# Optimization experiments

Measured on AMD Instinct MI355X. Metric: run time of the kernel, lower is better.

## Reference

```python
import jax, jax.numpy as jnp
import numpy as np

N = 20000   # nodes per type per hop
E = 200000  # edges per relation per hop
H = 512     # node_feature_hid_len
FU = 512    # raw user feature len
FI = 256    # raw item feature len
NUM_RES = 2
NUM_DNN = 2


def setup_inputs() -> dict:
    key = jax.random.key(0)
    ks = iter(jax.random.split(key, 64))
    p = lambda shape: jax.random.normal(next(ks), shape, dtype=jnp.float32) * 0.05
    inp = {}
    # features per hop per type
    for h in range(3):
        inp[f'feat_user_h{h}'] = jax.random.normal(next(ks), (N, FU), dtype=jnp.float32)
        inp[f'feat_item_h{h}'] = jax.random.normal(next(ks), (N, FI), dtype=jnp.float32)
    del inp['feat_user_h2_']; 


def _unused():
    pass

# rebuild setup_inputs cleanly (above stub replaced)

def setup_inputs() -> dict:
    key = jax.random.key(0)
    ks = iter(jax.random.split(key, 64))
    p = lambda shape: jax.random.normal(next(ks), shape, dtype=jnp.float32) * 0.05
    inp = {}
    for h in range(3):
        inp[f'feat_user_h{h}'] = jax.random.normal(next(ks), (N, FU), dtype=jnp.float32)
        inp[f'feat_item_h{h}'] = jax.random.normal(next(ks), (N, FI), dtype=jnp.float32)
    for name in ('edges_UI_h0', 'edges_IU_h0', 'edges_UI_h1', 'edges_IU_h1'):
        inp[name] = jax.random.randint(next(ks), (2, E), 0, N, dtype=jnp.int32)
    # per-node-type input transforms
    inp['W_user'] = p((FU, H)); inp['b_user'] = jnp.zeros((H,), jnp.float32)
    inp['W_item'] = p((FI, H)); inp['b_item'] = jnp.zeros((H,), jnp.float32)
    # per-relation GATConv params, stacked over 2 relations [UI, IU]
    inp['gat_feat_W'] = p((2, H, H)); inp['gat_feat_b'] = jnp.zeros((2, H), jnp.float32)
    inp['gat_att_w'] = p((2, 2 * H)); inp['gat_att_b'] = jnp.zeros((2,), jnp.float32)
    inp['gat_bias'] = jnp.zeros((2, H), jnp.float32)
    # Res_DNN params
    inp['prep_W'] = p((H, H)); inp['prep_b'] = jnp.zeros((H,), jnp.float32)
    inp['dnn_W'] = p((NUM_RES, NUM_DNN, H, H)); inp['dnn_b'] = jnp.zeros((NUM_RES, NUM_DNN, H), jnp.float32)
    inp['dnn_ln_g'] = jnp.ones((NUM_RES, NUM_DNN, H), jnp.float32); inp['dnn_ln_b'] = jnp.zeros((NUM_RES, NUM_DNN, H), jnp.float32)
    inp['res_ln_g'] = jnp.ones((NUM_RES, H), jnp.float32); inp['res_ln_b'] = jnp.zeros((NUM_RES, H), jnp.float32)
    inp['cls_W'] = p((H, 1)); inp['cls_b'] = jnp.zeros((1,), jnp.float32)
    return inp


def _ln(x, g, b, eps=1e-5):
    mu = jnp.mean(x, axis=-1, keepdims=True)
    var = jnp.mean((x - mu) ** 2, axis=-1, keepdims=True)
    return (x - mu) * jax.lax.rsqrt(var + eps) * g + b


def _gat(head_h, tail_h, edges, fW, fb, aw, ab, bias):
    # GATConv: feat_linear on both sides, tanh edge attention, per-source-row
    # sparse softmax, scatter-weighted sum of transformed tail features.
    s = head_h @ fW + fb            # [Nh, H]
    t = tail_h @ fW + fb            # [Nt, H]
    src, tgt = edges[0], edges[1]
    # att(cat([s_e, t_e])) split into per-node scores (same math as concat @ aw)
    e = jnp.tanh((s @ aw[:H])[src] + (t @ aw[H:])[tgt] + ab)  # [E]
    nh = head_h.shape[0]
    m = jax.ops.segment_max(e, src, num_segments=nh)
    ex = jnp.exp(e - m[src])
    den = jax.ops.segment_sum(ex, src, num_segments=nh)
    alpha = ex / den[src]
    hp = jax.ops.segment_sum(alpha[:, None] * t[tgt], src, num_segments=nh)
    return hp + bias


def _forward(feat_user_h0, feat_item_h0, feat_user_h1, feat_item_h1,
             feat_user_h2, feat_item_h2,
             W_user, b_user, W_item, b_item,
             gat_feat_W, gat_feat_b, gat_att_w, gat_att_b, gat_bias,
             prep_W, prep_b, dnn_W, dnn_b, dnn_ln_g, dnn_ln_b,
             res_ln_g, res_ln_b, cls_W, cls_b,
             edges_UI_h0, edges_IU_h0, edges_UI_h1, edges_IU_h1):
    def gat(r, head, tail, edges):
        return _gat(head, tail, edges, gat_feat_W[r], gat_feat_b[r],
                    gat_att_w[r], gat_att_b[r], gat_bias[r])
    # hop 2 (deepest): transformed source features
    su = feat_user_h2 @ W_user + b_user
    si = feat_item_h2 @ W_item + b_item
    # hop 1
    hu = feat_user_h1 @ W_user + b_user
    hi = feat_item_h1 @ W_item + b_item
    su_new = (hu + gat(0, hu, si, edges_UI_h1)) * 0.5  # mean of [self, UI agg]
    si_new = (hi + gat(1, hi, su, edges_IU_h1)) * 0.5
    su, si = su_new, si_new
    # hop 0
    hu = feat_user_h0 @ W_user + b_user
    hi = feat_item_h0 @ W_item + b_item
    su_new = (hu + gat(0, hu, si, edges_UI_h0)) * 0.5
    su = su_new  # target node type = 'user' (first key)
    # Res_DNN head
    x = su @ prep_W + prep_b
    for r in range(NUM_RES):
        sc = x
        for d in range(NUM_DNN):
            x = _ln(jnp.tanh(x @ dnn_W[r, d] + dnn_b[r, d]), dnn_ln_g[r, d], dnn_ln_b[r, d])
        x = _ln(jnp.tanh(sc + x), res_ln_g[r], res_ln_b[r])
    return jax.nn.sigmoid(x @ cls_W + cls_b)  # [N, 1]


def reference(feat_user_h0, feat_item_h0, feat_user_h1, feat_item_h1,
              feat_user_h2, feat_item_h2,
              edges_UI_h0, edges_IU_h0, edges_UI_h1, edges_IU_h1,
              W_user, b_user, W_item, b_item,
              gat_feat_W, gat_feat_b, gat_att_w, gat_att_b, gat_bias,
              prep_W, prep_b, dnn_W, dnn_b, dnn_ln_g, dnn_ln_b,
              res_ln_g, res_ln_b, cls_W, cls_b):
    return _forward(feat_user_h0, feat_item_h0, feat_user_h1, feat_item_h1,
                    feat_user_h2, feat_item_h2,
                    W_user, b_user, W_item, b_item,
                    gat_feat_W, gat_feat_b, gat_att_w, gat_att_b, gat_bias,
                    prep_W, prep_b, dnn_W, dnn_b, dnn_ln_g, dnn_ln_b,
                    res_ln_g, res_ln_b, cls_W, cls_b,
                    edges_UI_h0, edges_IU_h0, edges_UI_h1, edges_IU_h1)
```

## Files before the change

kernel.cpp:

```cpp
#include <hip/hip_runtime.h>
#include <math.h>

#define NN 20000
#define NE 200000
#define HH 512

typedef __attribute__((ext_vector_type(8))) short short8v;
typedef __attribute__((ext_vector_type(4))) float f32x4;

__device__ inline short f2bf(float f) {
    union { float f; unsigned u; } v; v.f = f;
    unsigned r = (v.u + 0x7fffu + ((v.u >> 16) & 1u)) >> 16;
    return (short)r;
}
__device__ inline float bf2f(short s) {
    union { unsigned u; float f; } v;
    v.u = ((unsigned)(unsigned short)s) << 16;
    return v.f;
}

__device__ inline void gload_lds16(const void* g, void* l) {
    __builtin_amdgcn_global_load_lds(
        (const __attribute__((address_space(1))) void*)g,
        (__attribute__((address_space(3))) void*)l, 16, 0, 0);
}

__global__ __launch_bounds__(256)
void wtr_all(const float* __restrict__ Wu, const float* __restrict__ Wi,
             const float* __restrict__ gfW, const float* __restrict__ prW,
             const float* __restrict__ dW,
             short* __restrict__ WTu, short* __restrict__ WTi,
             short* __restrict__ WTg0, short* __restrict__ WTg1,
             short* __restrict__ WTpr, short* __restrict__ WTd,
             short* __restrict__ WuB)
{
    __shared__ float t[32][33];
    int z = blockIdx.z;
    int by = blockIdx.y * 32;
    int bx = blockIdx.x * 32;
    int tx = threadIdx.x, ty = threadIdx.y;
    if (z == 9) {
        for (int i = ty; i < 32; i += 8)
            WuB[(size_t)(by + i) * 512 + bx + tx] =
                f2bf(Wu[(size_t)(by + i) * 512 + bx + tx]);
        return;
    }
    const float* src; short* dst; int K;
    if (z == 0)      { src = Wu;  dst = WTu;  K = 512; }
    else if (z == 1) { src = Wi;  dst = WTi;  K = 256; }
    else if (z == 2) { src = gfW; dst = WTg0; K = 512; }
    else if (z == 3) { src = gfW + (size_t)512 * 512; dst = WTg1; K = 512; }
    else if (z == 4) { src = prW; dst = WTpr; K = 512; }
    else { src = dW + (size_t)(z - 5) * 512 * 512;
           dst = WTd + (size_t)(z - 5) * 512 * 512; K = 512; }
    if (by >= K) return;
    for (int i = ty; i < 32; i += 8)
        t[i][tx] = src[(size_t)(by + i) * 512 + bx + tx];
    __syncthreads();
    for (int i = ty; i < 32; i += 8)
        dst[(size_t)(bx + i) * K + by + tx] = f2bf(t[tx][i]);
}

__global__ __launch_bounds__(256)
void mfma_lin(const short* __restrict__ X, const short* __restrict__ WT,
              const float* __restrict__ bias, float* __restrict__ outF,
              short* __restrict__ outB, int M, int K,
              const short* __restrict__ rdH, const short* __restrict__ rdT,
              const float* __restrict__ rduv, const float* __restrict__ rds0,
              float* __restrict__ rdss, float* __restrict__ rdts, int rdN)
{
    __shared__ short8v pool[4096];

    const int tid = threadIdx.x;
    const int lane = tid & 63;
    const int w = tid >> 6;

    const int nby = (M + 127) >> 7;
    const int nwg = nby << 2;
    int id = blockIdx.x;

    if (id >= nwg) {
        int row = (id - nwg) * 4 + w;
        if (!rdH || row >= rdN) return;
        short8v h = ((const short8v*)(rdH + (size_t)row * HH))[lane];
        short8v t = ((const short8v*)(rdT + (size_t)row * HH))[lane];
        const float4* up = (const float4*)rduv + lane * 2;
        const float4* vp = (const float4*)(rduv + HH) + lane * 2;
        float4 u0 = up[0], u1 = up[1], v0 = vp[0], v1 = vp[1];
        float a = bf2f(h[0])*u0.x + bf2f(h[1])*u0.y + bf2f(h[2])*u0.z + bf2f(h[3])*u0.w
                + bf2f(h[4])*u1.x + bf2f(h[5])*u1.y + bf2f(h[6])*u1.z + bf2f(h[7])*u1.w;
        float b = bf2f(t[0])*v0.x + bf2f(t[1])*v0.y + bf2f(t[2])*v0.z + bf2f(t[3])*v0.w
                + bf2f(t[4])*v1.x + bf2f(t[5])*v1.y + bf2f(t[6])*v1.z + bf2f(t[7])*v1.w;
#pragma unroll
        for (int m = 32; m >= 1; m >>= 1) {
            a += __shfl_xor(a, m);
            b += __shfl_xor(b, m);
        }
        if (lane == 0) { rdss[row] = a + rds0[0]; rdts[row] = b + rds0[1]; }
        return;
    }

    const int q = nwg >> 3, r = nwg & 7;
    int xcd = id & 7, wi = id >> 3;
    int wgid = (xcd < r ? xcd * (q + 1) : r * (q + 1) + (xcd - r) * q) + wi;
    const int col0 = (wgid & 3) * 128;
    const int row0 = (wgid >> 2) * 128;

    const int wr = (w >> 1) * 64;
    const int wc = (w & 1) * 64;

    const short* gsrc[8];
#pragma unroll
    for (int g = 0; g < 8; ++g) {
        int p = w * 512 + g * 64 + lane;
        if (p < 1024) {
            int row = p >> 3;
            int c = (p & 7) ^ (row & 7);
            int ga = row0 + row; if (ga >= M) ga = M - 1;
            gsrc[g] = X + (size_t)ga * K + c * 8;
        } else {
            int qq = p - 1024;
            int col = qq >> 3;
            int c = (qq & 7) ^ (col & 7);
            gsrc[g] = WT + (size_t)(col0 + col) * K + c * 8;
        }
    }

    int ar[2][4], br[2][4];
#pragma unroll
    for (int kk = 0; kk < 2; ++kk) {
#pragma unroll
        for (int i = 0; i < 4; ++i) {
            int rr = wr + i * 16 + (lane & 15);
            ar[kk][i] = rr * 8 + ((kk * 4 + (lane >> 4)) ^ (rr & 7));
            int nn = wc + i * 16 + (lane & 15);
            br[kk][i] = 1024 + nn * 8 + ((kk * 4 + (lane >> 4)) ^ (nn & 7));
        }
    }

    f32x4 acc[4][4];
#pragma unroll
    for (int i = 0; i < 4; ++i)
#pragma unroll
        for (int j = 0; j < 4; ++j)
            acc[i][j] = (f32x4){0.f, 0.f, 0.f, 0.f};

    auto stage = [&](int buf, int kk) {
        short8v* base = pool + buf * 2048 + w * 512;
#pragma unroll
        for (int g = 0; g < 8; ++g)
            gload_lds16(gsrc[g] + kk, base + g * 64);
    };

    const int nt = K >> 6;
    stage(0, 0);
    if (nt > 1) stage(1, 64);
    int cur = 0;
    for (int t = 0; t < nt; ++t) {
        if (t + 1 < nt) asm volatile("s_waitcnt vmcnt(8)" ::: "memory");
        else            asm volatile("s_waitcnt vmcnt(0)" ::: "memory");
        __builtin_amdgcn_s_barrier();
        const short8v* S = pool + cur * 2048;
#pragma unroll
        for (int kk = 0; kk < 2; ++kk) {
            short8v af[4], bf[4];
#pragma unroll
            for (int i = 0; i < 4; ++i) af[i] = S[ar[kk][i]];
#pragma unroll
            for (int j = 0; j < 4; ++j) bf[j] = S[br[kk][j]];
#pragma unroll
            for (int i = 0; i < 4; ++i)
#pragma unroll
                for (int j = 0; j < 4; ++j)
                    acc[i][j] = __builtin_amdgcn_mfma_f32_16x16x32_bf16(af[i], bf[j], acc[i][j], 0, 0, 0);
        }
        __builtin_amdgcn_s_barrier();
        if (t + 2 < nt) stage(cur, (t + 2) * 64);
        cur ^= 1;
    }

    float bj[4];
#pragma unroll
    for (int j = 0; j < 4; ++j)
        bj[j] = bias ? bias[col0 + wc + j * 16 + (lane & 15)] : 0.f;

    if (outF) {
#pragma unroll
        for (int i = 0; i < 4; ++i) {
#pragma unroll
            for (int rr = 0; rr < 4; ++rr) {
                int row = row0 + wr + i * 16 + (lane >> 4) * 4 + rr;
                if (row < M) {
                    float* op = outF + (size_t)row * HH + col0 + wc + (lane & 15);
#pragma unroll
                    for (int j = 0; j < 4; ++j) op[j * 16] = acc[i][j][rr] + bj[j];
                }
            }
        }
    }
    if (outB) {
        short* lt = (short*)pool;
#pragma unroll
        for (int i = 0; i < 4; ++i)
#pragma unroll
            for (int rr = 0; rr < 4; ++rr) {
                int lrow = wr + i * 16 + (lane >> 4) * 4 + rr;
#pragma unroll
                for (int j = 0; j < 4; ++j)
                    lt[lrow * 136 + wc + j * 16 + (lane & 15)] = f2bf(acc[i][j][rr] + bj[j]);
            }
        __syncthreads();
#pragma unroll
        for (int k = 0; k < 8; ++k) {
            int row = (tid >> 4) + 16 * k;
            int seg = tid & 15;
            int grow = row0 + row;
            if (grow < M) {
                short8v vv = *(short8v*)(lt + row * 136 + seg * 8);
                *(short8v*)(outB + (size_t)grow * HH + col0 + seg * 8) = vv;
            }
        }
    }
}

__global__ __launch_bounds__(256)
void mfma_linf(const float* __restrict__ XA, const float* __restrict__ XB2,
               int NA, const short* __restrict__ WT,
               const float* __restrict__ bias, short* __restrict__ outB,
               int M, int K,
               const short* __restrict__ rdH, const float* __restrict__ rdT32,
               const float* __restrict__ rdu, const float* __restrict__ rdwuv,
               const float* __restrict__ rdc, float* __restrict__ rdss,
               float* __restrict__ rdts, int rdN)
{
    __shared__ short8v pool[2304];

    const int tid = threadIdx.x;
    const int lane = tid & 63;
    const int w = tid >> 6;

    const int nby = (M + 127) >> 7;
    const int nwg = nby << 2;
    int id = blockIdx.x;

    if (id >= nwg) {
        int row = (id - nwg) * 4 + w;
        if (!rdH || row >= rdN) return;
        short8v h = ((const short8v*)(rdH + (size_t)row * HH))[lane];
        const float4* tp = (const float4*)(rdT32 + (size_t)row * HH) + lane * 2;
        float4 t0v = tp[0], t1v = tp[1];
        const float4* up = (const float4*)rdu + lane * 2;
        const float4* vp = (const float4*)rdwuv + lane * 2;
        float4 u0 = up[0], u1 = up[1], v0 = vp[0], v1 = vp[1];
        float a = bf2f(h[0])*u0.x + bf2f(h[1])*u0.y + bf2f(h[2])*u0.z + bf2f(h[3])*u0.w
                + bf2f(h[4])*u1.x + bf2f(h[5])*u1.y + bf2f(h[6])*u1.z + bf2f(h[7])*u1.w;
        float b = t0v.x*v0.x + t0v.y*v0.y + t0v.z*v0.z + t0v.w*v0.w
                + t1v.x*v1.x + t1v.y*v1.y + t1v.z*v1.z + t1v.w*v1.w;
#pragma unroll
        for (int m = 32; m >= 1; m >>= 1) {
            a += __shfl_xor(a, m);
            b += __shfl_xor(b, m);
        }
        if (lane == 0) { rdss[row] = a + rdc[0]; rdts[row] = b + rdc[1]; }
        return;
    }

    const int q = nwg >> 3, r = nwg & 7;
    int xcd = id & 7, wi = id >> 3;
    int wgid = (xcd < r ? xcd * (q + 1) : r * (q + 1) + (xcd - r) * q) + wi;
    const int col0 = (wgid & 3) * 128;
    const int row0 = (wgid >> 2) * 128;

    const int wr = (w >> 1) * 64;
    const int wc = (w & 1) * 64;

    const int srow = tid >> 1;
    const int sc0 = (tid & 1) * 2;
    int garow = row0 + srow; if (garow >= M) garow = M - 1;
    const float* abase = ((garow < NA) ? XA + (size_t)garow * K
                                       : XB2 + (size_t)(garow - NA) * K) + sc0 * 8;
    const int aswz = (srow >> 1) & 3;
    const int wi0 = srow * 4 + (sc0 ^ aswz);
    const int wi1 = srow * 4 + ((sc0 + 1) ^ aswz);

    const short* bsrc0; const short* bsrc1;
    int bbase0, bbase1;
    {
        int p0 = w * 128 + lane;
        int col = p0 >> 2;
        int c = (p0 & 3) ^ ((col >> 1) & 3);
        bsrc0 = WT + (size_t)(col0 + col) * K + c * 8;
        bbase0 = w * 128;
        int p1 = w * 128 + 64 + lane;
        col = p1 >> 2;
        c = (p1 & 3) ^ ((col >> 1) & 3);
        bsrc1 = WT + (size_t)(col0 + col) * K + c * 8;
        bbase1 = w * 128 + 64;
    }

    int ar[4], br[4];
#pragma unroll
    for (int i = 0; i < 4; ++i) {
        int rr = wr + i * 16 + (lane & 15);
        ar[i] = rr * 4 + ((lane >> 4) ^ ((rr >> 1) & 3));
        int nn = wc + i * 16 + (lane & 15);
        br[i] = 512 + nn * 4 + ((lane >> 4) ^ ((nn >> 1) & 3));
    }

    f32x4 acc[4][4];
#pragma unroll
    for (int i = 0; i < 4; ++i)
#pragma unroll
        for (int j = 0; j < 4; ++j)
            acc[i][j] = (f32x4){0.f, 0.f, 0.f, 0.f};

    const int nt = K >> 5;
    float4 rA0[4], rA1[4];

#define ISSUE_A(RA, T) {                                                   \
        const float4* p_ = (const float4*)(abase + (T) * 32);              \
        RA[0] = p_[0]; RA[1] = p_[1]; RA[2] = p_[2]; RA[3] = p_[3]; }
#define ISSUE_B(BUF, T) {                                                  \
        short8v* bb_ = pool + (BUF) * 1024 + 512;                          \
        gload_lds16(bsrc0 + (T) * 32, bb_ + bbase0);                       \
        gload_lds16(bsrc1 + (T) * 32, bb_ + bbase1); }
#define LINF_BODY(BUF, RA, T) {                                            \
        short8v s0_, s1_;                                                  \
        s0_[0]=f2bf(RA[0].x); s0_[1]=f2bf(RA[0].y); s0_[2]=f2bf(RA[0].z); s0_[3]=f2bf(RA[0].w); \
        s0_[4]=f2bf(RA[1].x); s0_[5]=f2bf(RA[1].y); s0_[6]=f2bf(RA[1].z); s0_[7]=f2bf(RA[1].w); \
        s1_[0]=f2bf(RA[2].x); s1_[1]=f2bf(RA[2].y); s1_[2]=f2bf(RA[2].z); s1_[3]=f2bf(RA[2].w); \
        s1_[4]=f2bf(RA[3].x); s1_[5]=f2bf(RA[3].y); s1_[6]=f2bf(RA[3].z); s1_[7]=f2bf(RA[3].w); \
        short8v* A_ = pool + (BUF) * 1024;                                 \
        A_[wi0] = s0_; A_[wi1] = s1_;                                      \
        if ((T) + 1 < nt) asm volatile("s_waitcnt vmcnt(6) lgkmcnt(0)" ::: "memory"); \
        else              asm volatile("s_waitcnt vmcnt(0) lgkmcnt(0)" ::: "memory"); \
        __builtin_amdgcn_s_barrier();                                      \
        const short8v* S_ = pool + (BUF) * 1024;                           \
        short8v af_[4], bf_[4];                                            \
        _Pragma("unroll")                                                  \
        for (int i_ = 0; i_ < 4; ++i_) af_[i_] = S_[ar[i_]];               \
        _Pragma("unroll")                                                  \
        for (int j_ = 0; j_ < 4; ++j_) bf_[j_] = S_[br[j_]];               \
        _Pragma("unroll")                                                  \
        for (int i_ = 0; i_ < 4; ++i_)                                     \
            _Pragma("unroll")                                              \
            for (int j_ = 0; j_ < 4; ++j_)                                 \
                acc[i_][j_] = __builtin_amdgcn_mfma_f32_16x16x32_bf16(af_[i_], bf_[j_], acc[i_][j_], 0, 0, 0); \
        __builtin_amdgcn_s_barrier();                                      \
        if ((T) + 2 < nt) { ISSUE_A(RA, (T) + 2); ISSUE_B(BUF, (T) + 2); } }

    ISSUE_A(rA0, 0);
    ISSUE_B(0, 0);
    ISSUE_A(rA1, 1);
    ISSUE_B(1, 1);
    for (int t = 0; t < nt; t += 2) {
        LINF_BODY(0, rA0, t);
        LINF_BODY(1, rA1, t + 1);
    }
#undef ISSUE_A
#undef ISSUE_B
#undef LINF_BODY

    float bj[4];
#pragma unroll
    for (int j = 0; j < 4; ++j)
        bj[j] = bias[col0 + wc + j * 16 + (lane & 15)];

    short* lt = (short*)pool;
#pragma unroll
    for (int i = 0; i < 4; ++i)
#pragma unroll
        for (int rr = 0; rr < 4; ++rr) {
            int lrow = wr + i * 16 + (lane >> 4) * 4 + rr;
#pragma unroll
            for (int j = 0; j < 4; ++j)
                lt[lrow * 136 + wc + j * 16 + (lane & 15)] = f2bf(acc[i][j][rr] + bj[j]);
        }
    __syncthreads();
#pragma unroll
    for (int k = 0; k < 8; ++k) {
        int row = (tid >> 4) + 16 * k;
        int seg = tid & 15;
        int grow = row0 + row;
        if (grow < M) {
            short8v vv = *(short8v*)(lt + row * 136 + seg * 8);
            *(short8v*)(outB + (size_t)grow * HH + col0 + seg * 8) = vv;
        }
    }
}

__global__ __launch_bounds__(256)
void gat_pre2(const float* __restrict__ gfW, const float* __restrict__ gfb,
              const float* __restrict__ gaw, float* __restrict__ uvall,
              float* __restrict__ s0t0all)
{
    int rrel = blockIdx.y;
    const float* fW = gfW + (size_t)rrel * HH * HH;
    const float* fb = gfb + rrel * HH;
    const float* aw = gaw + (size_t)rrel * 2 * HH;
    float* uv = uvall + rrel * 1024;
    float* s0t0 = s0t0all + rrel * 4;
    int row = blockIdx.x * 4 + (threadIdx.x >> 6);
    int lane = threadIdx.x & 63;
    const float4* ah = (const float4*)aw;
    const float4* at = (const float4*)(aw + HH);
    const float4* fp;
    if (row < 512)       fp = (const float4*)(fW + (size_t)row * HH);
    else if (row == 512) fp = (const float4*)fb;
    else return;
    float du = 0.f, dv = 0.f;
#pragma unroll
    for (int l = 0; l < 2; ++l) {
        int idx = lane * 2 + l;
        float4 f = fp[idx], a = ah[idx], b = at[idx];
        du += f.x*a.x + f.y*a.y + f.z*a.z + f.w*a.w;
        dv += f.x*b.x + f.y*b.y + f.z*b.z + f.w*b.w;
    }
#pragma unroll
    for (int m = 32; m >= 1; m >>= 1) {
        du += __shfl_xor(du, m);
        dv += __shfl_xor(dv, m);
    }
    if (lane == 0) {
        if (row < 512) { uv[row] = du; uv[512 + row] = dv; }
        else           { s0t0[0] = du; s0t0[1] = dv; }
    }
}

__global__ __launch_bounds__(256)
void wuvbc_kernel(const float* __restrict__ Wu, const float* __restrict__ bu,
                  const short* __restrict__ WTg1, const float* __restrict__ fb1,
                  const float* __restrict__ uvall, const float* __restrict__ s0t0a,
                  float* __restrict__ wuv, float* __restrict__ cpair,
                  float* __restrict__ bcomp)
{
    int row = blockIdx.x * 4 + (threadIdx.x >> 6);
    int lane = threadIdx.x & 63;
    if (blockIdx.y == 0) {
        const float* v1 = uvall + 1024 + 512;
        const float4* vp = (const float4*)v1 + lane * 2;
        float4 v0 = vp[0], v1v = vp[1];
        const float4* fp;
        if (row < 512)       fp = (const float4*)(Wu + (size_t)row * HH);
        else if (row == 512) fp = (const float4*)bu;
        else return;
        const float4* p = fp + lane * 2;
        float4 a = p[0], b = p[1];
        float d = a.x*v0.x + a.y*v0.y + a.z*v0.z + a.w*v0.w
                + b.x*v1v.x + b.y*v1v.y + b.z*v1v.z + b.w*v1v.w;
#pragma unroll
        for (int m = 32; m >= 1; m >>= 1) d += __shfl_xor(d, m);
        if (lane == 0) {
            if (row < 512) wuv[row] = d;
            else { cpair[0] = s0t0a[4]; cpair[1] = d + s0t0a[5]; }
        }
    } else {
        if (row >= 512) return;
        short8v wv8 = ((const short8v*)(WTg1 + (size_t)row * HH))[lane];
        const float4* bp = (const float4*)bu + lane * 2;
        float4 b0 = bp[0], b1 = bp[1];
        float d = bf2f(wv8[0])*b0.x + bf2f(wv8[1])*b0.y + bf2f(wv8[2])*b0.z + bf2f(wv8[3])*b0.w
                + bf2f(wv8[4])*b1.x + bf2f(wv8[5])*b1.y + bf2f(wv8[6])*b1.z + bf2f(wv8[7])*b1.w;
#pragma unroll
        for (int m = 32; m >= 1; m >>= 1) d += __shfl_xor(d, m);
        if (lane == 0) bcomp[row] = d + fb1[row];
    }
}

__global__ __launch_bounds__(256)
void count2_kernel(const int* __restrict__ s0, const int* __restrict__ s1,
                   int* __restrict__ c0, int* __restrict__ c1, int E)
{
    int i = blockIdx.x * blockDim.x + threadIdx.x;
    if (i < E) atomicAdd(&c0[s0[i]], 1);
    else if (i < 2 * E) atomicAdd(&c1[s1[i - E]], 1);
}

__global__ __launch_bounds__(1024)
void scan2_kernel(const int* __restrict__ c0, const int* __restrict__ c1,
                  int* __restrict__ o0, int* __restrict__ o1,
                  int* __restrict__ u0, int* __restrict__ u1, int n)
{
    const int* counts = blockIdx.x ? c1 : c0;
    int* offs = blockIdx.x ? o1 : o0;
    int* curs = blockIdx.x ? u1 : u0;
    __shared__ int part[1024];
    const int tid = threadIdx.x;
    const int CH = (n + 1023) / 1024;
    const int base = tid * CH;
    int s = 0;
    for (int i = 0; i < CH; ++i) {
        int idx = base + i;
        if (idx < n) s += counts[idx];
    }
    part[tid] = s;
    __syncthreads();
    for (int d = 1; d < 1024; d <<= 1) {
        int v = 0;
        if (tid >= d) v = part[tid - d];
        __syncthreads();
        if (tid >= d) part[tid] += v;
        __syncthreads();
    }
    int run = (tid == 0) ? 0 : part[tid - 1];
    for (int i = 0; i < CH; ++i) {
        int idx = base + i;
        if (idx < n) { offs[idx] = run; curs[idx] = run; run += counts[idx]; }
    }
    if (tid == 1023) offs[n] = run;
}

__global__ __launch_bounds__(256)
void fill_kernel(const int* __restrict__ src, const int* __restrict__ tgt,
                 const float* __restrict__ ss, const float* __restrict__ ts,
                 const float* __restrict__ ab_ptr, int* __restrict__ cursor,
                 int* __restrict__ tvals, float* __restrict__ wv,
                 int* __restrict__ eidx, int E)
{
    int i = blockIdx.x * blockDim.x + threadIdx.x;
    if (i >= E) return;
    int s = src[i], t = tgt[i];
    int pos = atomicAdd(&cursor[s], 1);
    tvals[pos] = t;
    wv[pos] = expf(tanhf(ss[s] + ts[t] + ab_ptr[0]));
    eidx[pos] = i;
}

__global__ __launch_bounds__(256)
void gat_agg_kernel(const int* __restrict__ offs, const int* __restrict__ tvals,
                    const float* __restrict__ wv, const int* __restrict__ eidx,
                    const short* __restrict__ T, const short* __restrict__ head,
                    const float* __restrict__ gbias, short* __restrict__ out, int N)
{
    __shared__ int   slt[4][512];
    __shared__ float slw[4][512];
    int w = threadIdx.x >> 6;
    int lane = threadIdx.x & 63;
    int s = blockIdx.x * 4 + w;
    if (s >= N) return;
    const int beg = offs[s], end = offs[s + 1];
    int L = end - beg;
    if (L > 512) L = 512;

    if (L <= 64) {
        int e = 0x7fffffff, t = 0; float fw = 0.f;
        if (lane < L) { e = eidx[beg + lane]; t = tvals[beg + lane]; fw = wv[beg + lane]; }
        int r = 0;
        for (int k = 0; k < L; ++k)
            r += (__shfl(e, k) < e) ? 1 : 0;
        if (lane < L) { slt[w][r] = t; slw[w][r] = fw; }
    } else {
        for (int j = lane; j < L; j += 64) {
            int e = eidx[beg + j];
            int r = 0;
            for (int k = 0; k < L; ++k) r += (eidx[beg + k] < e) ? 1 : 0;
            slt[w][r] = tvals[beg + j]; slw[w][r] = wv[beg + j];
        }
    }
    asm volatile("s_waitcnt lgkmcnt(0)" ::: "memory");

    float a[8];
#pragma unroll
    for (int q = 0; q < 8; ++q) a[q] = 0.f;
    float den = 0.f;

    int j = 0;
    for (; j + 8 <= L; j += 8) {
        short8v v[8];
        float wgt[8];
#pragma unroll
        for (int u = 0; u < 8; ++u) {
            wgt[u] = slw[w][j + u];
            v[u] = ((const short8v*)(T + (size_t)slt[w][j + u] * HH))[lane];
        }
#pragma unroll
        for (int u = 0; u < 8; ++u) {
            den += wgt[u];
#pragma unroll
            for (int q = 0; q < 8; ++q) a[q] = fmaf(wgt[u], bf2f(v[u][q]), a[q]);
        }
    }
    for (; j + 4 <= L; j += 4) {
        short8v v[4];
        float wgt[4];
#pragma unroll
        for (int u = 0; u < 4; ++u) {
            wgt[u] = slw[w][j + u];
            v[u] = ((const short8v*)(T + (size_t)slt[w][j + u] * HH))[lane];
        }
#pragma unroll
        for (int u = 0; u < 4; ++u) {
            den += wgt[u];
#pragma unroll
            for (int q = 0; q < 8; ++q) a[q] = fmaf(wgt[u], bf2f(v[u][q]), a[q]);
        }
    }
    for (; j < L; ++j) {
        float fw = slw[w][j];
        short8v tv = ((const short8v*)(T + (size_t)slt[w][j] * HH))[lane];
        den += fw;
#pragma unroll
        for (int q = 0; q < 8; ++q) a[q] = fmaf(fw, bf2f(tv[q]), a[q]);
    }
    float inv = (den > 0.f) ? 1.f / den : 0.f;

    short8v h = ((const short8v*)(head + (size_t)s * HH))[lane];
    const float4* bp = (const float4*)gbias + lane * 2;
    float4 b0 = bp[0], b1 = bp[1];
    float bb[8] = {b0.x, b0.y, b0.z, b0.w, b1.x, b1.y, b1.z, b1.w};
    short8v o;
#pragma unroll
    for (int q = 0; q < 8; ++q)
        o[q] = f2bf((bf2f(h[q]) + a[q] * inv + bb[q]) * 0.5f);
    ((short8v*)(out + (size_t)s * HH))[lane] = o;
}

__global__ __launch_bounds__(256)
void tanh_ln_kernel(const short* __restrict__ Z,
                    const float* __restrict__ g, const float* __restrict__ bta,
                    short* __restrict__ outB, int N)
{
    int row = blockIdx.x * 4 + (threadIdx.x >> 6);
    int lane = threadIdx.x & 63;
    if (row >= N) return;
    short8v zv = ((const short8v*)(Z + (size_t)row * HH))[lane];
    float v[8];
    float sum = 0.f, sum2 = 0.f;
#pragma unroll
    for (int q = 0; q < 8; ++q) {
        float t = tanhf(bf2f(zv[q]));
        v[q] = t; sum += t; sum2 = fmaf(t, t, sum2);
    }
#pragma unroll
    for (int m = 32; m >= 1; m >>= 1) {
        sum += __shfl_xor(sum, m); sum2 += __shfl_xor(sum2, m);
    }
    float mu = sum * (1.f/HH);
    float rs = rsqrtf(sum2 * (1.f/HH) - mu*mu + 1e-5f);
    const float4* gp = (const float4*)g + lane * 2;
    const float4* bp = (const float4*)bta + lane * 2;
    float4 g0 = gp[0], g1 = gp[1], c0 = bp[0], c1 = bp[1];
    float gg[8] = {g0.x, g0.y, g0.z, g0.w, g1.x, g1.y, g1.z, g1.w};
    float cc[8] = {c0.x, c0.y, c0.z, c0.w, c1.x, c1.y, c1.z, c1.w};
    short8v ob;
#pragma unroll
    for (int q = 0; q < 8; ++q) ob[q] = f2bf((v[q]-mu)*rs*gg[q] + cc[q]);
    ((short8v*)(outB + (size_t)row * HH))[lane] = ob;
}

__global__ __launch_bounds__(256)
void tanh_ln2_kernel(const short* __restrict__ Z, const float* __restrict__ sc,
                     const float* __restrict__ g1, const float* __restrict__ b1,
                     const float* __restrict__ g2, const float* __restrict__ b2,
                     short* __restrict__ outB, float* __restrict__ outF,
                     const float* __restrict__ cWp, const float* __restrict__ cbp,
                     float* __restrict__ outCls, int N)
{
    int row = blockIdx.x * 4 + (threadIdx.x >> 6);
    int lane = threadIdx.x & 63;
    if (row >= N) return;
    short8v zv = ((const short8v*)(Z + (size_t)row * HH))[lane];
    float v[8];
    float sum = 0.f, sum2 = 0.f;
#pragma unroll
    for (int q = 0; q < 8; ++q) {
        float t = tanhf(bf2f(zv[q]));
        v[q] = t; sum += t; sum2 = fmaf(t, t, sum2);
    }
#pragma unroll
    for (int m = 32; m >= 1; m >>= 1) {
        sum += __shfl_xor(sum, m); sum2 += __shfl_xor(sum2, m);
    }
    float mu = sum * (1.f/HH);
    float rs = rsqrtf(sum2 * (1.f/HH) - mu*mu + 1e-5f);
    {
        const float4* gp = (const float4*)g1 + lane * 2;
        const float4* bp = (const float4*)b1 + lane * 2;
        float4 g0 = gp[0], g1v = gp[1], c0 = bp[0], c1 = bp[1];
        float gg[8] = {g0.x, g0.y, g0.z, g0.w, g1v.x, g1v.y, g1v.z, g1v.w};
        float cc[8] = {c0.x, c0.y, c0.z, c0.w, c1.x, c1.y, c1.z, c1.w};
        const float4* sp = (const float4*)(sc + (size_t)row * HH) + lane * 2;
        float4 s0 = sp[0], s1 = sp[1];
        float ssv[8] = {s0.x, s0.y, s0.z, s0.w, s1.x, s1.y, s1.z, s1.w};
        sum = 0.f; sum2 = 0.f;
#pragma unroll
        for (int q = 0; q < 8; ++q) {
            float x2 = (v[q]-mu)*rs*gg[q] + cc[q];
            float t = tanhf(ssv[q] + x2);
            v[q] = t; sum += t; sum2 = fmaf(t, t, sum2);
        }
    }
#pragma unroll
    for (int m = 32; m >= 1; m >>= 1) {
        sum += __shfl_xor(sum, m); sum2 += __shfl_xor(sum2, m);
    }
    mu = sum * (1.f/HH);
    rs = rsqrtf(sum2 * (1.f/HH) - mu*mu + 1e-5f);
    const float4* gp = (const float4*)g2 + lane * 2;
    const float4* bp = (const float4*)b2 + lane * 2;
    float4 g0 = gp[0], g1v = gp[1], c0 = bp[0], c1 = bp[1];
    float gg[8] = {g0.x, g0.y, g0.z, g0.w, g1v.x, g1v.y, g1v.z, g1v.w};
    float cc[8] = {c0.x, c0.y, c0.z, c0.w, c1.x, c1.y, c1.z, c1.w};
    float o[8];
#pragma unroll
    for (int q = 0; q < 8; ++q) o[q] = (v[q]-mu)*rs*gg[q] + cc[q];
    if (outB) {
        short8v ob;
#pragma unroll
        for (int q = 0; q < 8; ++q) ob[q] = f2bf(o[q]);
        ((short8v*)(outB + (size_t)row * HH))[lane] = ob;
    }
    if (outF) {
        float4* op = (float4*)(outF + (size_t)row * HH) + lane * 2;
        op[0] = make_float4(o[0], o[1], o[2], o[3]);
        op[1] = make_float4(o[4], o[5], o[6], o[7]);
    }
    if (cWp) {
        const float4* wp = (const float4*)cWp + lane * 2;
        float4 w0 = wp[0], w1 = wp[1];
        float acc = o[0]*w0.x + o[1]*w0.y + o[2]*w0.z + o[3]*w0.w
                  + o[4]*w1.x + o[5]*w1.y + o[6]*w1.z + o[7]*w1.w;
#pragma unroll
        for (int m = 32; m >= 1; m >>= 1) acc += __shfl_xor(acc, m);
        if (lane == 0) outCls[row] = 1.f / (1.f + expf(-(acc + cbp[0])));
    }
}

extern "C" void kernel_launch(void* const* d_in, const int* in_sizes, int n_in,
                              void* d_out, int out_size, void* d_ws, size_t ws_size,
                              hipStream_t stream)
{
    (void)in_sizes; (void)n_in; (void)out_size; (void)ws_size;
    const int N = NN, E = NE, H = HH;
    const size_t NHf = (size_t)N * H;

    const float* fu0 = (const float*)d_in[0];
    const float* fi1 = (const float*)d_in[3];
    const float* fu2 = (const float*)d_in[4];
    const int* eUI0 = (const int*)d_in[6];
    const int* eIU1 = (const int*)d_in[9];
    const float* Wu  = (const float*)d_in[10];
    const float* bu  = (const float*)d_in[11];
    const float* Wi  = (const float*)d_in[12];
    const float* bi  = (const float*)d_in[13];
    const float* gfW = (const float*)d_in[14];
    const float* gfb = (const float*)d_in[15];
    const float* gaw = (const float*)d_in[16];
    const float* gab = (const float*)d_in[17];
    const float* gbias = (const float*)d_in[18];
    const float* prW = (const float*)d_in[19];
    const float* prb = (const float*)d_in[20];
    const float* dW  = (const float*)d_in[21];
    const float* db  = (const float*)d_in[22];
    const float* dlg = (const float*)d_in[23];
    const float* dlb = (const float*)d_in[24];
    const float* rlg = (const float*)d_in[25];
    const float* rlb = (const float*)d_in[26];
    const float* cW  = (const float*)d_in[27];
    const float* cb  = (const float*)d_in[28];

    float* B5     = (float*)d_ws;
    float* ssb    = B5 + NHf;
    float* tsb    = ssb + N;
    float* uvall  = tsb + N;
    float* s0t0a  = uvall + 2048;
    float* bcomp  = s0t0a + 8;
    float* wuv    = bcomp + 512;
    float* cpair  = wuv + 512;
    float* wvb    = cpair + 4;
    int* counts0 = (int*)(wvb + E);
    int* counts1 = counts0 + N;
    int* offs0   = counts1 + N;
    int* offs1   = offs0 + N + 1;
    int* cur0    = offs1 + N + 1;
    int* cur1    = cur0 + N;
    int* tvals   = cur1 + N;
    int* eidxb   = tvals + E;
    size_t boff = (size_t)((char*)(eidxb + E) - (char*)d_ws);
    boff = (boff + 15) & ~(size_t)15;
    short* HU0   = (short*)((char*)d_ws + boff);
    short* HI    = HU0 + NHf;
    short* SINEW = HI + NHf;
    short* T4    = SINEW + NHf;
    short* SUF   = T4 + NHf;
    short* ZBUF  = SUF + NHf;
    short* WTu   = ZBUF + NHf;
    short* WTi   = WTu + 512 * 512;
    short* WTg0  = WTi + 512 * 256;
    short* WTg1  = WTg0 + 512 * 512;
    short* WTpr  = WTg1 + 512 * 512;
    short* WTd   = WTpr + 512 * 512;
    short* WuB   = WTd + 4 * 512 * 512;
    short* WTcmp = WuB + 512 * 512;
    short* XB  = SINEW;
    short* ZB  = ZBUF;

    hipLaunchKernelGGL(wtr_all, dim3(16, 16, 10), dim3(32, 8), 0, stream,
                       Wu, Wi, gfW, prW, dW, WTu, WTi, WTg0, WTg1, WTpr, WTd, WuB);
    hipMemsetAsync(counts0, 0, 2 * N * sizeof(int), stream);
    hipLaunchKernelGGL(count2_kernel, dim3((2 * E + 255) / 256), dim3(256), 0, stream,
                       eUI0, eIU1, counts0, counts1, E);
    hipLaunchKernelGGL(scan2_kernel, dim3(2), dim3(1024), 0, stream,
                       counts0, counts1, offs0, offs1, cur0, cur1, N);
    hipLaunchKernelGGL(gat_pre2, dim3(130, 2), dim3(256), 0, stream,
                       gfW, gfb, gaw, uvall, s0t0a);
    hipLaunchKernelGGL(wuvbc_kernel, dim3(130, 2), dim3(256), 0, stream,
                       Wu, bu, WTg1, gfb + H, uvall, s0t0a, wuv, cpair, bcomp);
    hipLaunchKernelGGL(mfma_lin, dim3(16), dim3(256), 0, stream,
                       WTg1, WuB, (const float*)nullptr, (float*)nullptr, WTcmp,
                       512, 512, (const short*)nullptr, (const short*)nullptr,
                       (const float*)nullptr, (const float*)nullptr,
                       ssb, tsb, 0);

    const int rgrid = (N + 3) / 4;
    const int egrid = (E + 255) / 256;
    auto MLIN = [&](const short* X, const short* WT, const float* b,
                    float* oF, short* oB, int M, int K,
                    const short* rdH, const short* rdT, const float* rduv,
                    const float* rds0) {
        int nwg = ((M + 127) / 128) * 4;
        int grid = nwg + (rdH ? rgrid : 0);
        hipLaunchKernelGGL(mfma_lin, dim3(grid), dim3(256), 0, stream,
                           X, WT, b, oF, oB, M, K,
                           rdH, rdT, rduv, rds0, ssb, tsb, N);
    };
    auto MLINF = [&](const float* XA, const short* WT, const float* b,
                     short* oB, int M, int K,
                     const short* rdH, const float* rdT32, const float* rdu,
                     const float* rdwuv, const float* rdc) {
        int nwg = ((M + 127) / 128) * 4;
        int grid = nwg + (rdH ? rgrid : 0);
        hipLaunchKernelGGL(mfma_linf, dim3(grid), dim3(256), 0, stream,
                           XA, XA, M, WT, b, oB, M, K,
                           rdH, rdT32, rdu, rdwuv, rdc, ssb, tsb, N);
    };

    MLINF(fu0, WTu, bu, HU0, N, 512, nullptr, nullptr, nullptr, nullptr, nullptr);
    MLINF(fi1, WTi, bi, HI, N, 256, nullptr, nullptr, nullptr, nullptr, nullptr);

    MLINF(fu2, WTcmp, bcomp, T4, N, 512,
          HI, fu2, uvall + 1024, wuv, cpair);
    hipLaunchKernelGGL(fill_kernel, dim3(egrid), dim3(256), 0, stream,
                       eIU1, eIU1 + E, ssb, tsb, gab + 1, cur1, tvals, wvb,
                       eidxb, E);
    hipLaunchKernelGGL(gat_agg_kernel, dim3(rgrid), dim3(256), 0, stream,
                       offs1, tvals, wvb, eidxb, T4, HI, gbias + H, SINEW, N);

    MLIN(SINEW, WTg0, gfb, nullptr, T4, N, 512,
         HU0, SINEW, uvall, s0t0a);
    hipLaunchKernelGGL(fill_kernel, dim3(egrid), dim3(256), 0, stream,
                       eUI0, eUI0 + E, ssb, tsb, gab, cur0, tvals, wvb,
                       eidxb, E);
    hipLaunchKernelGGL(gat_agg_kernel, dim3(rgrid), dim3(256), 0, stream,
                       offs0, tvals, wvb, eidxb, T4, HU0, gbias, SUF, N);

    MLIN(SUF, WTpr, prb, B5, XB, N, 512, nullptr, nullptr, nullptr, nullptr);
    for (int r = 0; r < 2; ++r) {
        MLIN(XB, WTd + (size_t)(r * 2) * 512 * 512, db + (r * 2) * H,
             nullptr, ZB, N, 512, nullptr, nullptr, nullptr, nullptr);
        hipLaunchKernelGGL(tanh_ln_kernel, dim3(rgrid), dim3(256), 0, stream,
                           ZB, dlg + (r * 2) * H, dlb + (r * 2) * H, XB, N);
        MLIN(XB, WTd + (size_t)(r * 2 + 1) * 512 * 512, db + (r * 2 + 1) * H,
             nullptr, ZB, N, 512, nullptr, nullptr, nullptr, nullptr);
        if (r == 0) {
            hipLaunchKernelGGL(tanh_ln2_kernel, dim3(rgrid), dim3(256), 0, stream,
                               ZB, B5, dlg + H, dlb + H, rlg, rlb,
                               XB, B5, (const float*)nullptr, (const float*)nullptr,
                               (float*)nullptr, N);
        } else {
            hipLaunchKernelGGL(tanh_ln2_kernel, dim3(rgrid), dim3(256), 0, stream,
                               ZB, B5, dlg + 3 * H, dlb + 3 * H, rlg + H, rlb + H,
                               (short*)nullptr, (float*)nullptr, cW, cb,
                               (float*)d_out, N);
        }
    }
}
```

Baseline: 496.7 us.

## Merge three input projections into one launch and fold score weights algebraically

The three fp32-input GEMMs (user hop0, item hop1, composed user hop2) now run in a single multi-segment kernel launch instead of three separate launches. The attention score reductions no longer read the bf16 projected outputs (HI, HU0). They use the raw fp32 features dotted with precomputed folded vectors (W·u plus bias constants) built in an extended wuvbc2 kernel. This removes the dependency on GEMM outputs so all three GEMMs and the score rows can share one grid, cutting launch gaps and tail effects. In exchange, the scores come from fp32 features rather than rounded bf16 projections, which slightly changes their numerics.

```diff
diff --git a/kernel.cpp b/kernel.cpp
--- a/kernel.cpp
+++ b/kernel.cpp
@@ -65,9 +65,10 @@
 void mfma_lin(const short* __restrict__ X, const short* __restrict__ WT,
               const float* __restrict__ bias, float* __restrict__ outF,
               short* __restrict__ outB, int M, int K,
-              const short* __restrict__ rdH, const short* __restrict__ rdT,
-              const float* __restrict__ rduv, const float* __restrict__ rds0,
-              float* __restrict__ rdss, float* __restrict__ rdts, int rdN)
+              const float* __restrict__ rdF, const float* __restrict__ rdfv,
+              const short* __restrict__ rdB, const float* __restrict__ rdbv,
+              const float* __restrict__ rdc, float* __restrict__ rdss,
+              float* __restrict__ rdts, int rdN)
 {
     __shared__ short8v pool[4096];
 
@@ -81,14 +82,16 @@
 
     if (id >= nwg) {
         int row = (id - nwg) * 4 + w;
-        if (!rdH || row >= rdN) return;
-        short8v h = ((const short8v*)(rdH + (size_t)row * HH))[lane];
-        short8v t = ((const short8v*)(rdT + (size_t)row * HH))[lane];
-        const float4* up = (const float4*)rduv + lane * 2;
-        const float4* vp = (const float4*)(rduv + HH) + lane * 2;
-        float4 u0 = up[0], u1 = up[1], v0 = vp[0], v1 = vp[1];
-        float a = bf2f(h[0])*u0.x + bf2f(h[1])*u0.y + bf2f(h[2])*u0.z + bf2f(h[3])*u0.w
-                + bf2f(h[4])*u1.x + bf2f(h[5])*u1.y + bf2f(h[6])*u1.z + bf2f(h[7])*u1.w;
+        if (!rdF || row >= rdN) return;
+        const float4* fp = (const float4*)(rdF + (size_t)row * HH) + lane * 2;
+        float4 f0 = fp[0], f1 = fp[1];
+        const float4* up = (const float4*)rdfv + lane * 2;
+        float4 u0 = up[0], u1 = up[1];
+        float a = f0.x*u0.x + f0.y*u0.y + f0.z*u0.z + f0.w*u0.w
+                + f1.x*u1.x + f1.y*u1.y + f1.z*u1.z + f1.w*u1.w;
+        short8v t = ((const short8v*)(rdB + (size_t)row * HH))[lane];
+        const float4* vp = (const float4*)rdbv + lane * 2;
+        float4 v0 = vp[0], v1 = vp[1];
         float b = bf2f(t[0])*v0.x + bf2f(t[1])*v0.y + bf2f(t[2])*v0.z + bf2f(t[3])*v0.w
                 + bf2f(t[4])*v1.x + bf2f(t[5])*v1.y + bf2f(t[6])*v1.z + bf2f(t[7])*v1.w;
 #pragma unroll
@@ -96,7 +99,7 @@
             a += __shfl_xor(a, m);
             b += __shfl_xor(b, m);
         }
-        if (lane == 0) { rdss[row] = a + rds0[0]; rdts[row] = b + rds0[1]; }
+        if (lane == 0) { rdss[row] = a + rdc[0]; rdts[row] = b + rdc[1]; }
         return;
     }
 
@@ -224,14 +227,17 @@
 }
 
 __global__ __launch_bounds__(256)
-void mfma_linf(const float* __restrict__ XA, const float* __restrict__ XB2,
-               int NA, const short* __restrict__ WT,
-               const float* __restrict__ bias, short* __restrict__ outB,
-               int M, int K,
-               const short* __restrict__ rdH, const float* __restrict__ rdT32,
-               const float* __restrict__ rdu, const float* __restrict__ rdwuv,
-               const float* __restrict__ rdc, float* __restrict__ rdss,
-               float* __restrict__ rdts, int rdN)
+void mfma_multi(const float* __restrict__ A0, const short* __restrict__ W0,
+                const float* __restrict__ b0, short* __restrict__ O0,
+                const float* __restrict__ A1, const short* __restrict__ W1,
+                const float* __restrict__ b1, short* __restrict__ O1,
+                const float* __restrict__ A2, const short* __restrict__ W2,
+                const float* __restrict__ b2, short* __restrict__ O2,
+                int M,
+                const float* __restrict__ rdF1, const float* __restrict__ rdv1,
+                const float* __restrict__ rdF2, const float* __restrict__ rdv2,
+                const float* __restrict__ rdc, float* __restrict__ rdss,
+                float* __restrict__ rdts, int rdN)
 {
     __shared__ short8v pool[2304];
 
@@ -243,17 +249,18 @@
     const int nwg = nby << 2;
     int id = blockIdx.x;
 
-    if (id >= nwg) {
-        int row = (id - nwg) * 4 + w;
-        if (!rdH || row >= rdN) return;
-        short8v h = ((const short8v*)(rdH + (size_t)row * HH))[lane];
-        const float4* tp = (const float4*)(rdT32 + (size_t)row * HH) + lane * 2;
+    if (id >= 3 * nwg) {
+        int row = (id - 3 * nwg) * 4 + w;
+        if (row >= rdN) return;
+        const float4* fp = (const float4*)(rdF1 + (size_t)row * 256) + lane;
+        float4 f = fp[0];
+        const float4* u1p = (const float4*)rdv1 + lane;
+        float4 u1 = u1p[0];
+        float a = f.x*u1.x + f.y*u1.y + f.z*u1.z + f.w*u1.w;
+        const float4* tp = (const float4*)(rdF2 + (size_t)row * HH) + lane * 2;
         float4 t0v = tp[0], t1v = tp[1];
-        const float4* up = (const float4*)rdu + lane * 2;
-        const float4* vp = (const float4*)rdwuv + lane * 2;
-        float4 u0 = up[0], u1 = up[1], v0 = vp[0], v1 = vp[1];
-        float a = bf2f(h[0])*u0.x + bf2f(h[1])*u0.y + bf2f(h[2])*u0.z + bf2f(h[3])*u0.w
-                + bf2f(h[4])*u1.x + bf2f(h[5])*u1.y + bf2f(h[6])*u1.z + bf2f(h[7])*u1.w;
+        const float4* vp = (const float4*)rdv2 + lane * 2;
+        float4 v0 = vp[0], v1 = vp[1];
         float b = t0v.x*v0.x + t0v.y*v0.y + t0v.z*v0.z + t0v.w*v0.w
                 + t1v.x*v1.x + t1v.y*v1.y + t1v.z*v1.z + t1v.w*v1.w;
 #pragma unroll
@@ -265,8 +272,16 @@
         return;
     }
 
+    int seg = id / nwg;
+    int sid = id - seg * nwg;
+    const float* XA = (seg == 0) ? A0 : ((seg == 1) ? A1 : A2);
+    const short* WT = (seg == 0) ? W0 : ((seg == 1) ? W1 : W2);
+    const float* bias = (seg == 0) ? b0 : ((seg == 1) ? b1 : b2);
+    short* outB = (seg == 0) ? O0 : ((seg == 1) ? O1 : O2);
+    const int K = (seg == 1) ? 256 : 512;
+
     const int q = nwg >> 3, r = nwg & 7;
-    int xcd = id & 7, wi = id >> 3;
+    int xcd = sid & 7, wi = sid >> 3;
     int wgid = (xcd < r ? xcd * (q + 1) : r * (q + 1) + (xcd - r) * q) + wi;
     const int col0 = (wgid & 3) * 128;
     const int row0 = (wgid >> 2) * 128;
@@ -277,8 +292,7 @@
     const int srow = tid >> 1;
     const int sc0 = (tid & 1) * 2;
     int garow = row0 + srow; if (garow >= M) garow = M - 1;
-    const float* abase = ((garow < NA) ? XA + (size_t)garow * K
-                                       : XB2 + (size_t)(garow - NA) * K) + sc0 * 8;
+    const float* abase = XA + (size_t)garow * K + sc0 * 8;
     const int aswz = (srow >> 1) & 3;
     const int wi0 = srow * 4 + (sc0 ^ aswz);
     const int wi1 = srow * 4 + ((sc0 + 1) ^ aswz);
@@ -380,11 +394,11 @@
 #pragma unroll
     for (int k = 0; k < 8; ++k) {
         int row = (tid >> 4) + 16 * k;
-        int seg = tid & 15;
+        int seg2 = tid & 15;
         int grow = row0 + row;
         if (grow < M) {
-            short8v vv = *(short8v*)(lt + row * 136 + seg * 8);
-            *(short8v*)(outB + (size_t)grow * HH + col0 + seg * 8) = vv;
+            short8v vv = *(short8v*)(lt + row * 136 + seg2 * 8);
+            *(short8v*)(outB + (size_t)grow * HH + col0 + seg2 * 8) = vv;
         }
     }
 }
@@ -428,17 +442,20 @@
 }
 
 __global__ __launch_bounds__(256)
-void wuvbc_kernel(const float* __restrict__ Wu, const float* __restrict__ bu,
-                  const short* __restrict__ WTg1, const float* __restrict__ fb1,
-                  const float* __restrict__ uvall, const float* __restrict__ s0t0a,
-                  float* __restrict__ wuv, float* __restrict__ cpair,
-                  float* __restrict__ bcomp)
+void wuvbc2_kernel(const float* __restrict__ Wu, const float* __restrict__ bu,
+                   const float* __restrict__ Wi, const float* __restrict__ bi,
+                   const short* __restrict__ WTg1, const float* __restrict__ fb1,
+                   const float* __restrict__ uvall, const float* __restrict__ s0t0a,
+                   float* __restrict__ wuv, float* __restrict__ cpair1,
+                   float* __restrict__ bcomp, float* __restrict__ wiu,
+                   float* __restrict__ wuu0, float* __restrict__ cpair0)
 {
     int row = blockIdx.x * 4 + (threadIdx.x >> 6);
     int lane = threadIdx.x & 63;
-    if (blockIdx.y == 0) {
-        const float* v1 = uvall + 1024 + 512;
-        const float4* vp = (const float4*)v1 + lane * 2;
+    int y = blockIdx.y;
+    if (y == 0 || y == 3) {
+        const float* vec = (y == 0) ? (uvall + 1024 + 512) : (uvall + 0);
+        const float4* vp = (const float4*)vec + lane * 2;
         float4 v0 = vp[0], v1v = vp[1];
         const float4* fp;
         if (row < 512)       fp = (const float4*)(Wu + (size_t)row * HH);
@@ -451,10 +468,15 @@
 #pragma unroll
         for (int m = 32; m >= 1; m >>= 1) d += __shfl_xor(d, m);
         if (lane == 0) {
-            if (row < 512) wuv[row] = d;
-            else { cpair[0] = s0t0a[4]; cpair[1] = d + s0t0a[5]; }
-        }
-    } else {
+            if (y == 0) {
+                if (row < 512) wuv[row] = d;
+                else           cpair1[1] = d + s0t0a[5];
+            } else {
+                if (row < 512) wuu0[row] = d;
+                else { cpair0[0] = d + s0t0a[0]; cpair0[1] = s0t0a[1]; }
+            }
+        }
+    } else if (y == 1) {
         if (row >= 512) return;
         short8v wv8 = ((const short8v*)(WTg1 + (size_t)row * HH))[lane];
         const float4* bp = (const float4*)bu + lane * 2;
@@ -464,6 +486,24 @@
 #pragma unroll
         for (int m = 32; m >= 1; m >>= 1) d += __shfl_xor(d, m);
         if (lane == 0) bcomp[row] = d + fb1[row];
+    } else {
+        const float* u1 = uvall + 1024;
+        const float4* vp = (const float4*)u1 + lane * 2;
+        float4 v0 = vp[0], v1v = vp[1];
+        const float4* fp;
+        if (row < 256)       fp = (const float4*)(Wi + (size_t)row * HH);
+        else if (row == 256) fp = (const float4*)bi;
+        else return;
+        const float4* p = fp + lane * 2;
+        float4 a = p[0], b = p[1];
+        float d = a.x*v0.x + a.y*v0.y + a.z*v0.z + a.w*v0.w
+                + b.x*v1v.x + b.y*v1v.y + b.z*v1v.z + b.w*v1v.w;
+#pragma unroll
+        for (int m = 32; m >= 1; m >>= 1) d += __shfl_xor(d, m);
+        if (lane == 0) {
+            if (row < 256) wiu[row] = d;
+            else           cpair1[0] = d + s0t0a[4];
+        }
     }
 }
 
@@ -766,8 +806,11 @@
     float* s0t0a  = uvall + 2048;
     float* bcomp  = s0t0a + 8;
     float* wuv    = bcomp + 512;
-    float* cpair  = wuv + 512;
-    float* wvb    = cpair + 4;
+    float* wiu    = wuv + 512;
+    float* wuu0   = wiu + 512;
+    float* cpair1 = wuu0 + 512;
+    float* cpair0 = cpair1 + 4;
+    float* wvb    = cpair0 + 4;
     int* counts0 = (int*)(wvb + E);
     int* counts1 = counts0 + N;
     int* offs0   = counts1 + N;
@@ -804,64 +847,60 @@
                        counts0, counts1, offs0, offs1, cur0, cur1, N);
     hipLaunchKernelGGL(gat_pre2, dim3(130, 2), dim3(256), 0, stream,
                        gfW, gfb, gaw, uvall, s0t0a);
-    hipLaunchKernelGGL(wuvbc_kernel, dim3(130, 2), dim3(256), 0, stream,
-                       Wu, bu, WTg1, gfb + H, uvall, s0t0a, wuv, cpair, bcomp);
+    hipLaunchKernelGGL(wuvbc2_kernel, dim3(130, 4), dim3(256), 0, stream,
+                       Wu, bu, Wi, bi, WTg1, gfb + H, uvall, s0t0a,
+                       wuv, cpair1, bcomp, wiu, wuu0, cpair0);
     hipLaunchKernelGGL(mfma_lin, dim3(16), dim3(256), 0, stream,
                        WTg1, WuB, (const float*)nullptr, (float*)nullptr, WTcmp,
-                       512, 512, (const short*)nullptr, (const short*)nullptr,
-                       (const float*)nullptr, (const float*)nullptr,
-                       ssb, tsb, 0);
+                       512, 512, (const float*)nullptr, (const float*)nullptr,
+                       (const short*)nullptr, (const float*)nullptr,
+                       (const float*)nullptr, ssb, tsb, 0);
 
     const int rgrid = (N + 3) / 4;
     const int egrid = (E + 255) / 256;
-    auto MLIN = [&](const short* X, const short* WT, const float* b,
-                    float* oF, short* oB, int M, int K,
-                    const short* rdH, const short* rdT, const float* rduv,
-                    const float* rds0) {
-        int nwg = ((M + 127) / 128) * 4;
-        int grid = nwg + (rdH ? rgrid : 0);
-        hipLaunchKernelGGL(mfma_lin, dim3(grid), dim3(256), 0, stream,
-                           X, WT, b, oF, oB, M, K,
-                           rdH, rdT, rduv, rds0, ssb, tsb, N);
-    };
-    auto MLINF = [&](const float* XA, const short* WT, const float* b,
-                     short* oB, int M, int K,
-                     const short* rdH, const float* rdT32, const float* rdu,
-                     const float* rdwuv, const float* rdc) {
-        int nwg = ((M + 127) / 128) * 4;
-        int grid = nwg + (rdH ? rgrid : 0);
-        hipLaunchKernelGGL(mfma_linf, dim3(grid), dim3(256), 0, stream,
-                           XA, XA, M, WT, b, oB, M, K,
-                           rdH, rdT32, rdu, rdwuv, rdc, ssb, tsb, N);
-    };
-
-    MLINF(fu0, WTu, bu, HU0, N, 512, nullptr, nullptr, nullptr, nullptr, nullptr);
-    MLINF(fi1, WTi, bi, HI, N, 256, nullptr, nullptr, nullptr, nullptr, nullptr);
-
-    MLINF(fu2, WTcmp, bcomp, T4, N, 512,
-          HI, fu2, uvall + 1024, wuv, cpair);
+    const int nwg = ((N + 127) / 128) * 4;
+
+    hipLaunchKernelGGL(mfma_multi, dim3(3 * nwg + rgrid), dim3(256), 0, stream,
+                       fu0, WTu, bu, HU0,
+                       fi1, WTi, bi, HI,
+                       fu2, WTcmp, bcomp, T4,
+                       N, fi1, wiu, fu2, wuv, cpair1, ssb, tsb, N);
+
     hipLaunchKernelGGL(fill_kernel, dim3(egrid), dim3(256), 0, stream,
                        eIU1, eIU1 + E, ssb, tsb, gab + 1, cur1, tvals, wvb,
                        eidxb, E);
     hipLaunchKernelGGL(gat_agg_kernel, dim3(rgrid), dim3(256), 0, stream,
                        offs1, tvals, wvb, eidxb, T4, HI, gbias + H, SINEW, N);
 
-    MLIN(SINEW, WTg0, gfb, nullptr, T4, N, 512,
-         HU0, SINEW, uvall, s0t0a);
+    hipLaunchKernelGGL(mfma_lin, dim3(nwg + rgrid), dim3(256), 0, stream,
+                       SINEW, WTg0, gfb, (float*)nullptr, T4, N, 512,
+                       fu0, wuu0, SINEW, uvall + 512, cpair0, ssb, tsb, N);
     hipLaunchKernelGGL(fill_kernel, dim3(egrid), dim3(256), 0, stream,
                        eUI0, eUI0 + E, ssb, tsb, gab, cur0, tvals, wvb,
                        eidxb, E);
     hipLaunchKernelGGL(gat_agg_kernel, dim3(rgrid), dim3(256), 0, stream,
                        offs0, tvals, wvb, eidxb, T4, HU0, gbias, SUF, N);
 
-    MLIN(SUF, WTpr, prb, B5, XB, N, 512, nullptr, nullptr, nullptr, nullptr);
+    hipLaunchKernelGGL(mfma_lin, dim3(nwg), dim3(256), 0, stream,
+                       SUF, WTpr, prb, B5, XB, N, 512,
+                       (const float*)nullptr, (const float*)nullptr,
+                       (const short*)nullptr, (const float*)nullptr,
+                       (const float*)nullptr, ssb, tsb, 0);
     for (int r = 0; r < 2; ++r) {
-        MLIN(XB, WTd + (size_t)(r * 2) * 512 * 512, db + (r * 2) * H,
-             nullptr, ZB, N, 512, nullptr, nullptr, nullptr, nullptr);
+        hipLaunchKernelGGL(mfma_lin, dim3(nwg), dim3(256), 0, stream,
+                           XB, WTd + (size_t)(r * 2) * 512 * 512, db + (r * 2) * H,
+                           (float*)nullptr, ZB, N, 512,
+                           (const float*)nullptr, (const float*)nullptr,
+                           (const short*)nullptr, (const float*)nullptr,
+                           (const float*)nullptr, ssb, tsb, 0);
         hipLaunchKernelGGL(tanh_ln_kernel, dim3(rgrid), dim3(256), 0, stream,
                            ZB, dlg + (r * 2) * H, dlb + (r * 2) * H, XB, N);
-        MLIN(XB, WTd + (size_t)(r * 2 + 1) * 512 * 512, db + (r * 2 + 1) * H,
-             nullptr, ZB, N, 512, nullptr, nullptr, nullptr, nullptr);
+        hipLaunchKernelGGL(mfma_lin, dim3(nwg), dim3(256), 0, stream,
+                           XB, WTd + (size_t)(r * 2 + 1) * 512 * 512, db + (r * 2 + 1) * H,
+                           (float*)nullptr, ZB, N, 512,
+                           (const float*)nullptr, (const float*)nullptr,
+                           (const short*)nullptr, (const float*)nullptr,
+                           (const float*)nullptr, ssb, tsb, 0);
         if (r == 0) {
             hipLaunchKernelGGL(tanh_ln2_kernel, dim3(rgrid), dim3(256), 0, stream,
                                ZB, B5, dlg + H, dlb + H, rlg, rlb,
```

Measured after the change: 493.4 us (median of 2 runs). About the same (-0.7%).
